# Optimization experiments

Measured on AMD Instinct MI355X. Metric: run time of the kernel, lower is better.

The kernel has to match this reference:

```python
import jax, jax.numpy as jnp
import numpy as np
from jax import lax

B, K, Z, C, H, W = 32, 7, 64, 3, 64, 64
G = H + 6  # decoder grid for 'small' variant
ITERS = 3
SCALE = Z ** -0.5
EPS = 1e-8


def _pe(h, w):
    # matches SlotAttention.create_positional_embedding: shape [w, h, 4]
    ww = jnp.linspace(0.0, 1.0, w)
    hh = jnp.linspace(0.0, 1.0, h)
    a = jnp.broadcast_to((1.0 - ww)[:, None], (w, h))  # dist_right
    b = jnp.broadcast_to(ww[:, None], (w, h))          # dist_left
    c = jnp.broadcast_to(hh[None, :], (w, h))          # dist_top
    d = jnp.broadcast_to((1.0 - hh)[None, :], (w, h))  # dist_bottom
    return jnp.stack([a, b, c, d], -1)


def _ln(x, g, b):
    m = x.mean(-1, keepdims=True)
    v = ((x - m) ** 2).mean(-1, keepdims=True)
    return (x - m) * lax.rsqrt(v + 1e-5) * g + b


def _conv(x, w, b, p):
    y = lax.conv_general_dilated(x, w, (1, 1), [(p, p), (p, p)],
                                 dimension_numbers=('NCHW', 'OIHW', 'NCHW'))
    return y + b[None, :, None, None]


def setup_inputs() -> dict:
    key = jax.random.key(0)
    ks = iter(jax.random.split(key, 64))
    nrm = lambda shape, s=0.05: jax.random.normal(next(ks), shape, jnp.float32) * s
    d = {}
    d['inputs'] = jax.random.normal(next(ks), (B, C, H, W), jnp.float32)
    d['noise'] = jax.random.normal(next(ks), (B * K, Z), jnp.float32)
    d['enc_pos_w'] = nrm((4, 64)); d['enc_pos_b'] = jnp.zeros(64, jnp.float32)
    d['ec1_w'] = nrm((64, 3, 5, 5)); d['ec1_b'] = jnp.zeros(64, jnp.float32)
    d['ec2_w'] = nrm((64, 64, 5, 5)); d['ec2_b'] = jnp.zeros(64, jnp.float32)
    d['ec3_w'] = nrm((64, 64, 5, 5)); d['ec3_b'] = jnp.zeros(64, jnp.float32)
    d['ec4_w'] = nrm((64, 64, 5, 5)); d['ec4_b'] = jnp.zeros(64, jnp.float32)
    d['ln1_g'] = jnp.ones(64, jnp.float32); d['ln1_b'] = jnp.zeros(64, jnp.float32)
    d['fc1_w'] = nrm((64, 64)); d['fc1_b'] = jnp.zeros(64, jnp.float32)
    d['fc2_w'] = nrm((64, 64)); d['fc2_b'] = jnp.zeros(64, jnp.float32)
    d['lns_g'] = jnp.ones(Z, jnp.float32); d['lns_b'] = jnp.zeros(Z, jnp.float32)
    d['lnf_g'] = jnp.ones(Z, jnp.float32); d['lnf_b'] = jnp.zeros(Z, jnp.float32)
    d['q_w'] = nrm((Z, Z)); d['k_w'] = nrm((64, Z)); d['v_w'] = nrm((64, Z))
    d['mlp1_w'] = nrm((Z, 128)); d['mlp1_b'] = jnp.zeros(128, jnp.float32)
    d['mlp2_w'] = nrm((128, Z)); d['mlp2_b'] = jnp.zeros(Z, jnp.float32)
    d['gru_wih'] = nrm((3 * Z, Z)); d['gru_whh'] = nrm((3 * Z, Z))
    d['gru_bih'] = jnp.zeros(3 * Z, jnp.float32); d['gru_bhh'] = jnp.zeros(3 * Z, jnp.float32)
    d['init_slots'] = jnp.concatenate([jnp.zeros((1, Z), jnp.float32), jnp.ones((1, Z), jnp.float32)], 1)
    d['dec_pos_w'] = nrm((4, Z)); d['dec_pos_b'] = jnp.zeros(Z, jnp.float32)
    d['dc1_w'] = nrm((32, Z, 5, 5)); d['dc1_b'] = jnp.zeros(32, jnp.float32)
    d['dc2_w'] = nrm((32, 32, 5, 5)); d['dc2_b'] = jnp.zeros(32, jnp.float32)
    d['dc3_w'] = nrm((32, 32, 5, 5)); d['dc3_b'] = jnp.zeros(32, jnp.float32)
    d['dc4_w'] = nrm((4, 32, 3, 3)); d['dc4_b'] = jnp.zeros(4, jnp.float32)
    return d


def _forward(inputs, noise, enc_pos_w, enc_pos_b, ec1_w, ec1_b, ec2_w, ec2_b,
             ec3_w, ec3_b, ec4_w, ec4_b, ln1_g, ln1_b, fc1_w, fc1_b, fc2_w, fc2_b,
             lns_g, lns_b, lnf_g, lnf_b, q_w, k_w, v_w, mlp1_w, mlp1_b, mlp2_w,
             mlp2_b, gru_wih, gru_whh, gru_bih, gru_bhh, init_slots, dec_pos_w,
             dec_pos_b, dc1_w, dc1_b, dc2_w, dc2_b, dc3_w, dc3_b, dc4_w, dc4_b):
    # ---- encoder ----
    h = jax.nn.relu(_conv(inputs, ec1_w, ec1_b, 2))
    h = jax.nn.relu(_conv(h, ec2_w, ec2_b, 2))
    h = jax.nn.relu(_conv(h, ec3_w, ec3_b, 2))
    h = jax.nn.relu(_conv(h, ec4_w, ec4_b, 2))
    h = h.transpose(0, 2, 3, 1)                        # [B,H,W,64]
    pe = _pe(H, W) @ enc_pos_w + enc_pos_b             # [W,H,64] (H==W)
    h = h + pe[None]
    feat = h.reshape(B, H * W, 64)
    feat = _ln(feat, ln1_g, ln1_b)
    feat = jax.nn.relu(feat @ fc1_w + fc1_b) @ fc2_w + fc2_b
    k = feat @ k_w                                     # [B,N,Z]
    v = feat @ v_w
    # ---- slot init: Normal(loc, softplus(sp)).rsample() ----
    loc, sp = jnp.split(init_slots, 2, axis=1)
    slots = (loc + jax.nn.softplus(sp) * noise).reshape(B, K, Z)
    # ---- iterative slot attention ----
    for _ in range(ITERS):
        prev = slots
        q = (_ln(prev, lns_g, lns_b) @ q_w) * SCALE
        dots = jnp.einsum('bid,bjd->bij', q, k)        # [B,K,N]
        attn = jax.nn.softmax(dots, axis=1) + EPS      # normalize over slots
        attn = attn / attn.sum(-1, keepdims=True)      # renormalize over keys
        updates = jnp.einsum('bjd,bij->bid', v, attn)  # [B,K,Z]
        # GRU cell (single step), torch gate order r,z,n
        gi = updates.reshape(-1, Z) @ gru_wih.T + gru_bih
        gh = prev.reshape(-1, Z) @ gru_whh.T + gru_bhh
        ir, iz, inn = jnp.split(gi, 3, -1)
        hr, hz, hn = jnp.split(gh, 3, -1)
        r = jax.nn.sigmoid(ir + hr)
        zg = jax.nn.sigmoid(iz + hz)
        n = jnp.tanh(inn + r * hn)
        slots = ((1.0 - zg) * n + zg * prev.reshape(-1, Z)).reshape(B, K, Z)
        slots = slots + (jax.nn.relu(_ln(slots, lnf_g, lnf_b) @ mlp1_w + mlp1_b) @ mlp2_w + mlp2_b)
    # ---- spatial-broadcast decoder ('small') ----
    flat = slots.reshape(B * K, Z)
    zb = jnp.broadcast_to(flat[:, :, None, None], (B * K, Z, G, G))
    pe_d = (_pe(G, G) @ dec_pos_w + dec_pos_b).transpose(2, 0, 1)  # [Z,G,G]
    zb = zb + pe_d[None]
    o = jax.nn.relu(_conv(zb, dc1_w, dc1_b, 1))        # 70->68
    o = jax.nn.relu(_conv(o, dc2_w, dc2_b, 1))         # 68->66
    o = jax.nn.relu(_conv(o, dc3_w, dc3_b, 1))         # 66->64
    o = _conv(o, dc4_w, dc4_b, 1)                      # 64->64, 4ch
    x_loc = jax.nn.sigmoid(o[:, :3]).reshape(B, K, C, H, W)
    mask_logits = o[:, 3].reshape(B, K, 1, H, W)
    mask_logp = jax.nn.log_softmax(mask_logits, axis=1)
    x_orig = (inputs + 1.0) / 2.0
    recon = (x_loc * jnp.exp(mask_logp)).sum(1)
    mse = ((x_orig - recon) ** 2).sum() / B
    return mse, x_loc, mask_logp, slots


def reference(inputs, noise, enc_pos_w, enc_pos_b, ec1_w, ec1_b, ec2_w, ec2_b,
              ec3_w, ec3_b, ec4_w, ec4_b, ln1_g, ln1_b, fc1_w, fc1_b, fc2_w, fc2_b,
              lns_g, lns_b, lnf_g, lnf_b, q_w, k_w, v_w, mlp1_w, mlp1_b, mlp2_w,
              mlp2_b, gru_wih, gru_whh, gru_bih, gru_bhh, init_slots, dec_pos_w,
              dec_pos_b, dc1_w, dc1_b, dc2_w, dc2_b, dc3_w, dc3_b, dc4_w, dc4_b):
    return _forward(inputs, noise, enc_pos_w, enc_pos_b, ec1_w, ec1_b, ec2_w, ec2_b,
                    ec3_w, ec3_b, ec4_w, ec4_b, ln1_g, ln1_b, fc1_w, fc1_b, fc2_w, fc2_b,
                    lns_g, lns_b, lnf_g, lnf_b, q_w, k_w, v_w, mlp1_w, mlp1_b, mlp2_w,
                    mlp2_b, gru_wih, gru_whh, gru_bih, gru_bhh, init_slots, dec_pos_w,
                    dec_pos_b, dc1_w, dc1_b, dc2_w, dc2_b, dc3_w, dc3_b, dc4_w, dc4_b)
```

## Files before the change

### kernel.cpp

```cpp
#include <hip/hip_runtime.h>
#include <math.h>

typedef short bf16x8 __attribute__((ext_vector_type(8)));
typedef float f32x4 __attribute__((ext_vector_type(4)));

#define WS_B0   0u
#define WS_B1   4194304u
#define WS_K    8388608u
#define WS_V    16777216u
#define WS_ATTN 25165824u
#define WS_PART 26083328u
#define WS_SLOT 26327040u
#define WS_ROW  26341376u
#define SCALE_ 0.125f

#define OFF_PEB   0u
#define OFF_WCLS  160000u
#define OFF_S     180000u
#define OFF_ZB    250000u

__device__ __forceinline__ float wave_sum(float v) {
#pragma unroll
    for (int m = 32; m >= 1; m >>= 1) v += __shfl_xor(v, m, 64);
    return v;
}
__device__ __forceinline__ unsigned short f2bf(float f) {
    unsigned u = __float_as_uint(f);
    u = u + 0x7fffu + ((u >> 16) & 1u);
    return (unsigned short)(u >> 16);
}
__device__ __forceinline__ float bf2f(unsigned short h) {
    return __uint_as_float(((unsigned)h) << 16);
}

__global__ __launch_bounds__(256) void pack_weights(
    const float* __restrict__ w, unsigned short* __restrict__ wp,
    int CIN, int COUT_STORE, int KS, int NT, int total)
{
    int t = blockIdx.x * 256 + threadIdx.x;
    if (t >= total) return;
    int lane = t & 63;
    int nt = (t >> 6) % NT;
    int ch = t / (64 * NT);
    int CPT = CIN / 32;
    int cic = ch % CPT;
    int tap = ch / CPT;
    int ky = tap / KS, kx = tap % KS;
    int co = nt * 16 + (lane & 15);
    int k0 = cic * 32 + (lane >> 4) * 8;
    unsigned short v[8];
#pragma unroll
    for (int j = 0; j < 8; ++j) {
        int ci = k0 + j;
        float f = (co < COUT_STORE) ? w[((size_t)(co * CIN + ci) * KS + ky) * KS + kx] : 0.f;
        v[j] = f2bf(f);
    }
    *(uint4*)(wp + (size_t)t * 8) = *(uint4*)v;
}

__global__ __launch_bounds__(256) void pack_fc(
    const float* __restrict__ w, unsigned short* __restrict__ wp)
{
    int t = blockIdx.x * 256 + threadIdx.x;
    if (t >= 512) return;
    int lane = t & 63;
    int nt = (t >> 6) & 3;
    int ck = t >> 8;
    int n = nt * 16 + (lane & 15);
    int k0 = ck * 32 + (lane >> 4) * 8;
    unsigned short v[8];
#pragma unroll
    for (int j = 0; j < 8; ++j) v[j] = f2bf(w[(size_t)(k0 + j) * 64 + n]);
    *(uint4*)(wp + (size_t)t * 8) = *(uint4*)v;
}

template<int CIN, int COUT, int KS, int PAD, int NSTORE, int RELU, int OUTF32>
__global__ __launch_bounds__(256) void conv_mfma(
    const unsigned short* __restrict__ in, const unsigned short* __restrict__ wpack,
    const float* __restrict__ bias, void* __restrict__ outv,
    int Hin, int Win, int Hout, int Wout, int tilesX, int tilesY)
{
    constexpr int TS = 16, TH = TS + KS - 1;
    constexpr int NT = COUT / 16;
    constexpr int CPT = CIN / 32;
    constexpr int G8 = CIN / 8;
    __shared__ __align__(16) unsigned short tile[TH][TH][CIN];
    const int tpb = tilesX * tilesY;
    const int n = blockIdx.x / tpb;
    const int t = blockIdx.x % tpb;
    const int ty0 = (t / tilesX) * TS, tx0 = (t % tilesX) * TS;
    const int tid = threadIdx.x;

    const unsigned short* inb = in + (size_t)n * Hin * Win * CIN;
    for (int idx = tid; idx < TH * TH * G8; idx += 256) {
        int g = idx % G8;
        int c = (idx / G8) % TH;
        int r = idx / (G8 * TH);
        int iy = ty0 - PAD + r, ix = tx0 - PAD + c;
        uint4 vv = make_uint4(0, 0, 0, 0);
        if (iy >= 0 && iy < Hin && ix >= 0 && ix < Win)
            vv = *(const uint4*)(inb + ((size_t)iy * Win + ix) * CIN + g * 8);
        int slot = (g * 8 + c * 8) % CIN;
        *(uint4*)&tile[r][c][slot] = vv;
    }
    __syncthreads();

    const int wv = tid >> 6, lane = tid & 63;
    const int q = lane >> 4, m = lane & 15;
    const int row0 = wv * 4;
    f32x4 acc[4][NT];
#pragma unroll
    for (int mt = 0; mt < 4; ++mt)
#pragma unroll
        for (int nt = 0; nt < NT; ++nt) acc[mt][nt] = (f32x4){0.f, 0.f, 0.f, 0.f};

#pragma unroll
    for (int cic = 0; cic < CPT; ++cic) {
#pragma unroll
        for (int kx = 0; kx < KS; ++kx) {
            bf16x8 B[KS][NT];
#pragma unroll
            for (int ky = 0; ky < KS; ++ky)
#pragma unroll
                for (int nt = 0; nt < NT; ++nt)
                    B[ky][nt] = *(const bf16x8*)(wpack +
                        ((size_t)(((ky * KS + kx) * CPT + cic) * NT + nt) * 64 + lane) * 8);
            const int cbase = m + kx;
            const int slot = (cic * 32 + q * 8 + cbase * 8) % CIN;
#pragma unroll
            for (int ir = 0; ir < KS + 3; ++ir) {
                bf16x8 afr = *(const bf16x8*)&tile[row0 + ir][cbase][slot];
#pragma unroll
                for (int ky = 0; ky < KS; ++ky) {
                    const int mt = ir - ky;
                    if (mt < 0 || mt > 3) continue;
#pragma unroll
                    for (int nt = 0; nt < NT; ++nt)
                        acc[mt][nt] = __builtin_amdgcn_mfma_f32_16x16x32_bf16(afr, B[ky][nt], acc[mt][nt], 0, 0, 0);
                }
            }
        }
    }

#pragma unroll
    for (int nt = 0; nt < NT; ++nt) {
        const int co = nt * 16 + m;
        const float bv = (co < NSTORE) ? bias[co] : 0.f;
#pragma unroll
        for (int mt = 0; mt < 4; ++mt) {
            const int oy = ty0 + wv * 4 + mt;
#pragma unroll
            for (int j = 0; j < 4; ++j) {
                const int ox = tx0 + q * 4 + j;
                if (oy < Hout && ox < Wout && co < NSTORE) {
                    float v = acc[mt][nt][j] + bv;
                    if (RELU) v = fmaxf(v, 0.f);
                    size_t o = (((size_t)n * Hout + oy) * Wout + ox) * NSTORE + co;
                    if (OUTF32) ((float*)outv)[o] = v;
                    else ((unsigned short*)outv)[o] = f2bf(v);
                }
            }
        }
    }
}

__global__ __launch_bounds__(256) void pe_synth(
    const float* __restrict__ dpw, const float* __restrict__ dpb,
    unsigned short* __restrict__ peb, float* __restrict__ zbias)
{
    const int tid = threadIdx.x;
    if (blockIdx.x == 0 && tid < 32) zbias[tid] = 0.f;
    const int pix = blockIdx.x * 256 + tid;
    if (pix >= 4900) return;
    const int iy = pix / 70, ix = pix % 70;
    const float fy = iy * (1.f / 69.f), fx = ix * (1.f / 69.f);
    unsigned short v[64];
#pragma unroll
    for (int ci = 0; ci < 64; ++ci) {
        float p = (1.f - fy) * dpw[ci] + fy * dpw[64 + ci]
                + fx * dpw[128 + ci] + (1.f - fx) * dpw[192 + ci] + dpb[ci];
        v[ci] = f2bf(p);
    }
    uint4* ob = (uint4*)(peb + (size_t)pix * 64);
#pragma unroll
    for (int i = 0; i < 8; ++i) ob[i] = ((uint4*)v)[i];
}

__global__ __launch_bounds__(256) void wcls_build(
    const float* __restrict__ w, float* __restrict__ wcls)
{
    int idx = blockIdx.x * 256 + threadIdx.x;
    if (idx >= 9 * 32 * 64) return;
    int cls = idx / (32 * 64);
    int co = (idx / 64) % 32;
    int ci = idx % 64;
    int rc = cls / 3, cc = cls % 3;
    int ky0 = (rc == 0) ? 1 : 0, ky1 = (rc == 2) ? 3 : 4;
    int kx0 = (cc == 0) ? 1 : 0, kx1 = (cc == 2) ? 3 : 4;
    float s = 0.f;
    const float* wb = w + (size_t)(co * 64 + ci) * 25;
    for (int ky = ky0; ky <= ky1; ++ky)
        for (int kx = kx0; kx <= kx1; ++kx)
            s += wb[ky * 5 + kx];
    wcls[idx] = s;
}

__global__ __launch_bounds__(256) void slot_s(
    const float* __restrict__ slots, const float* __restrict__ wcls,
    float* __restrict__ S)
{
    int idx = blockIdx.x * 256 + threadIdx.x;
    if (idx >= 224 * 9 * 32) return;
    int n = idx / (9 * 32);
    int cls = (idx / 32) % 9;
    int co = idx % 32;
    const float* sl = slots + n * 64;
    const float* wc = wcls + (size_t)(cls * 32 + co) * 64;
    float s = 0.f;
#pragma unroll
    for (int ci = 0; ci < 64; ++ci) s = fmaf(sl[ci], wc[ci], s);
    S[idx] = s;
}

__global__ __launch_bounds__(256) void dc1_assemble(
    const float* __restrict__ P, const float* __restrict__ S,
    const float* __restrict__ bias, int n0,
    unsigned short* __restrict__ out)
{
    const int gid = blockIdx.x * 256 + threadIdx.x;
    const int nl = gid / 4624;
    const int pix = gid % 4624;
    const int oy = pix / 68, ox = pix % 68;
    const int rc = (oy == 0) ? 0 : ((oy == 67) ? 2 : 1);
    const int cc = (ox == 0) ? 0 : ((ox == 67) ? 2 : 1);
    const float* Sp = S + ((size_t)(n0 + nl) * 9 + (rc * 3 + cc)) * 32;
    const float* Pp = P + (size_t)pix * 32;
    unsigned short v[32];
#pragma unroll
    for (int co = 0; co < 32; ++co)
        v[co] = f2bf(fmaxf(bias[co] + Pp[co] + Sp[co], 0.f));
    uint4* ob = (uint4*)(out + ((size_t)nl * 4624 + pix) * 32);
#pragma unroll
    for (int i = 0; i < 4; ++i) ob[i] = ((uint4*)v)[i];
}

__global__ __launch_bounds__(256) void conv_ec1(
    const float* __restrict__ in, const float* __restrict__ wts,
    const float* __restrict__ bias, unsigned short* __restrict__ out)
{
    __shared__ float tile[3][20][21];
    const int blk = blockIdx.x;
    const int n = blk >> 6;
    const int sub = blk & 63;
    const int t = sub >> 2;
    const int cog = sub & 3;
    const int ty0 = (t >> 2) * 16, tx0 = (t & 3) * 16;
    const int tid = threadIdx.x;
    for (int idx = tid; idx < 1200; idx += 256) {
        int ci = idx / 400, rc = idx % 400;
        int r = rc / 20, c = rc % 20;
        int gy = ty0 + r - 2, gx = tx0 + c - 2;
        float v = 0.f;
        if (gy >= 0 && gy < 64 && gx >= 0 && gx < 64)
            v = in[((size_t)n * 3 + ci) * 4096 + gy * 64 + gx];
        tile[ci][r][c] = v;
    }
    __syncthreads();
    const int lx = tid & 15, ly = tid >> 4;
    float acc[16];
#pragma unroll
    for (int co = 0; co < 16; ++co) acc[co] = bias[cog * 16 + co];
    for (int ci = 0; ci < 3; ++ci) {
        float val[25];
#pragma unroll
        for (int ky = 0; ky < 5; ++ky)
#pragma unroll
            for (int kx = 0; kx < 5; ++kx) val[ky * 5 + kx] = tile[ci][ly + ky][lx + kx];
#pragma unroll
        for (int co = 0; co < 16; ++co) {
            const float* wc = wts + (size_t)((cog * 16 + co) * 3 + ci) * 25;
            float a = acc[co];
#pragma unroll
            for (int tt = 0; tt < 25; ++tt) a = fmaf(val[tt], wc[tt], a);
            acc[co] = a;
        }
    }
    unsigned short tmp[16];
#pragma unroll
    for (int co = 0; co < 16; ++co) tmp[co] = f2bf(fmaxf(acc[co], 0.f));
    uint4* ob = (uint4*)(out + (((size_t)n * 64 + ty0 + ly) * 64 + tx0 + lx) * 64 + cog * 16);
    ob[0] = ((uint4*)tmp)[0];
    ob[1] = ((uint4*)tmp)[1];
}

__global__ __launch_bounds__(256) void encoder_tail_mfma(
    const unsigned short* __restrict__ h4,
    const float* __restrict__ epw, const float* __restrict__ epb,
    const float* __restrict__ ln1g, const float* __restrict__ ln1b,
    const unsigned short* __restrict__ pfc1, const float* __restrict__ fc1b,
    const unsigned short* __restrict__ pfc2, const float* __restrict__ fc2b,
    const unsigned short* __restrict__ pkw, const unsigned short* __restrict__ pvw,
    unsigned short* __restrict__ kout, unsigned short* __restrict__ vout)
{
    __shared__ __align__(16) unsigned short X[64][72];
    const int b = blockIdx.x >> 6;
    const int y = blockIdx.x & 63;
    const int tid = threadIdx.x;

    {
        const int p = tid >> 2, sub = tid & 3;
        const unsigned short* hp = h4 + ((((size_t)b * 64 + y) * 64 + p) * 64) + sub * 16;
        unsigned short raw[16];
        *(uint4*)(raw)     = *(const uint4*)hp;
        *(uint4*)(raw + 8) = *(const uint4*)(hp + 8);
        const float fy = y * (1.f / 63.f), fx = p * (1.f / 63.f);
        float f[16];
        float s1 = 0.f, s2 = 0.f;
#pragma unroll
        for (int j = 0; j < 16; ++j) {
            int ch = sub * 16 + j;
            float pe = (1.f - fy) * epw[ch] + fy * epw[64 + ch]
                     + fx * epw[128 + ch] + (1.f - fx) * epw[192 + ch] + epb[ch];
            float v = bf2f(raw[j]) + pe;
            f[j] = v;
            s1 += v;
            s2 += v * v;
        }
        s1 += __shfl_xor(s1, 1, 64); s1 += __shfl_xor(s1, 2, 64);
        s2 += __shfl_xor(s2, 1, 64); s2 += __shfl_xor(s2, 2, 64);
        const float m = s1 * (1.f / 64.f);
        const float var = s2 * (1.f / 64.f) - m * m;
        const float inv = rsqrtf(var + 1e-5f);
        unsigned short xb[16];
#pragma unroll
        for (int j = 0; j < 16; ++j) {
            int ch = sub * 16 + j;
            xb[j] = f2bf((f[j] - m) * inv * ln1g[ch] + ln1b[ch]);
        }
        *(uint4*)&X[p][sub * 16]     = ((uint4*)xb)[0];
        *(uint4*)&X[p][sub * 16 + 8] = ((uint4*)xb)[1];
    }
    __syncthreads();

    const int w = tid >> 6, lane = tid & 63;
    const int q = lane >> 4, m_ = lane & 15;
    const int row0 = w * 16;

    {
        f32x4 a1[4];
#pragma unroll
        for (int nt = 0; nt < 4; ++nt) a1[nt] = (f32x4){0.f, 0.f, 0.f, 0.f};
#pragma unroll
        for (int ck = 0; ck < 2; ++ck) {
            bf16x8 afr = *(const bf16x8*)&X[row0 + m_][ck * 32 + q * 8];
#pragma unroll
            for (int nt = 0; nt < 4; ++nt) {
                bf16x8 bfr = *(const bf16x8*)(pfc1 + ((size_t)((ck * 4 + nt) * 64 + lane)) * 8);
                a1[nt] = __builtin_amdgcn_mfma_f32_16x16x32_bf16(afr, bfr, a1[nt], 0, 0, 0);
            }
        }
        __syncthreads();
#pragma unroll
        for (int nt = 0; nt < 4; ++nt) {
            const float bb = fc1b[nt * 16 + m_];
#pragma unroll
            for (int reg = 0; reg < 4; ++reg)
                X[row0 + q * 4 + reg][nt * 16 + m_] = f2bf(fmaxf(a1[nt][reg] + bb, 0.f));
        }
    }
    __syncthreads();

    {
        f32x4 a2[4];
#pragma unroll
        for (int nt = 0; nt < 4; ++nt) a2[nt] = (f32x4){0.f, 0.f, 0.f, 0.f};
#pragma unroll
        for (int ck = 0; ck < 2; ++ck) {
            bf16x8 afr = *(const bf16x8*)&X[row0 + m_][ck * 32 + q * 8];
#pragma unroll
            for (int nt = 0; nt < 4; ++nt) {
                bf16x8 bfr = *(const bf16x8*)(pfc2 + ((size_t)((ck * 4 + nt) * 64 + lane)) * 8);
                a2[nt] = __builtin_amdgcn_mfma_f32_16x16x32_bf16(afr, bfr, a2[nt], 0, 0, 0);
            }
        }
        __syncthreads();
#pragma unroll
        for (int nt = 0; nt < 4; ++nt) {
            const float bb = fc2b[nt * 16 + m_];
#pragma unroll
            for (int reg = 0; reg < 4; ++reg)
                X[row0 + q * 4 + reg][nt * 16 + m_] = f2bf(a2[nt][reg] + bb);
        }
    }
    __syncthreads();

    {
        f32x4 ak[4], av[4];
#pragma unroll
        for (int nt = 0; nt < 4; ++nt) {
            ak[nt] = (f32x4){0.f, 0.f, 0.f, 0.f};
            av[nt] = (f32x4){0.f, 0.f, 0.f, 0.f};
        }
#pragma unroll
        for (int ck = 0; ck < 2; ++ck) {
            bf16x8 afr = *(const bf16x8*)&X[row0 + m_][ck * 32 + q * 8];
#pragma unroll
            for (int nt = 0; nt < 4; ++nt) {
                bf16x8 bk = *(const bf16x8*)(pkw + ((size_t)((ck * 4 + nt) * 64 + lane)) * 8);
                bf16x8 bv = *(const bf16x8*)(pvw + ((size_t)((ck * 4 + nt) * 64 + lane)) * 8);
                ak[nt] = __builtin_amdgcn_mfma_f32_16x16x32_bf16(afr, bk, ak[nt], 0, 0, 0);
                av[nt] = __builtin_amdgcn_mfma_f32_16x16x32_bf16(afr, bv, av[nt], 0, 0, 0);
            }
        }
        const size_t base = ((size_t)b * 4096) + y * 64 + row0;
#pragma unroll
        for (int nt = 0; nt < 4; ++nt) {
            const int ch = nt * 16 + m_;
#pragma unroll
            for (int reg = 0; reg < 4; ++reg) {
                const size_t o = (base + q * 4 + reg) * 64 + ch;
                kout[o] = f2bf(ak[nt][reg]);
                vout[o] = f2bf(av[nt][reg]);
            }
        }
    }
}

__global__ __launch_bounds__(256) void slot_init(
    const float* __restrict__ noise, const float* __restrict__ init_slots,
    float* __restrict__ slots, float* __restrict__ rowsum)
{
    int i = blockIdx.x * 256 + threadIdx.x;
    if (i < 224) rowsum[i] = 0.f;
    if (i < 224 * 64) {
        int z = i & 63;
        float spl = log1pf(expf(init_slots[64 + z]));
        slots[i] = init_slots[z] + spl * noise[i];
    }
}

__global__ __launch_bounds__(256) void attn_pass1(
    const unsigned short* __restrict__ kbuf, const float* __restrict__ slots,
    const float* __restrict__ lnsg, const float* __restrict__ lnsb,
    const float* __restrict__ qw,
    float* __restrict__ attn, float* __restrict__ rowsum)
{
    __shared__ float qs[7][64];
    __shared__ float red[7][4];
    const int b = blockIdx.x >> 4;
    const int jb = (blockIdx.x & 15) * 256;
    const int tid = threadIdx.x;
    const int lane = tid & 63, wv = tid >> 6;
    for (int i = wv; i < 7; i += 4) {
        float s = slots[(b * 7 + i) * 64 + lane];
        float m = wave_sum(s) * (1.f / 64.f);
        float d = s - m;
        float var = wave_sum(d * d) * (1.f / 64.f);
        float x = d * rsqrtf(var + 1e-5f) * lnsg[lane] + lnsb[lane];
        float qv = 0.f;
        for (int c = 0; c < 64; ++c) qv = fmaf(__shfl(x, c, 64), qw[c * 64 + lane], qv);
        qs[i][lane] = qv * SCALE_;
    }
    __syncthreads();
    const int j = jb + tid;
    float kr[64];
    const unsigned short* kp = kbuf + (((size_t)b * 4096) + j) * 64;
#pragma unroll
    for (int d8 = 0; d8 < 8; ++d8) {
        uint4 kv = ((const uint4*)kp)[d8];
        const unsigned short* h = (const unsigned short*)&kv;
#pragma unroll
        for (int z = 0; z < 8; ++z) kr[d8 * 8 + z] = bf2f(h[z]);
    }
    float dots[7];
#pragma unroll
    for (int i = 0; i < 7; ++i) {
        float a = 0.f;
#pragma unroll
        for (int d = 0; d < 64; ++d) a = fmaf(kr[d], qs[i][d], a);
        dots[i] = a;
    }
    float mx = dots[0];
#pragma unroll
    for (int i = 1; i < 7; ++i) mx = fmaxf(mx, dots[i]);
    float sum = 0.f;
#pragma unroll
    for (int i = 0; i < 7; ++i) { dots[i] = expf(dots[i] - mx); sum += dots[i]; }
    const float inv = 1.f / sum;
#pragma unroll
    for (int i = 0; i < 7; ++i) {
        float a = dots[i] * inv + 1e-8f;
        dots[i] = a;
        attn[(((size_t)b * 7) + i) * 4096 + j] = a;
    }
#pragma unroll
    for (int i = 0; i < 7; ++i) {
        float s = wave_sum(dots[i]);
        if (lane == 0) red[i][wv] = s;
    }
    __syncthreads();
    if (tid < 7) {
        float s = red[tid][0] + red[tid][1] + red[tid][2] + red[tid][3];
        atomicAdd(&rowsum[b * 7 + tid], s);
    }
}

__global__ __launch_bounds__(256) void attn_pass2(
    const unsigned short* __restrict__ vbuf, const float* __restrict__ attn,
    float* __restrict__ part)
{
    const int b = blockIdx.x >> 4;
    const int js = blockIdx.x & 15;
    const int tid = threadIdx.x;
    const int d = tid & 63, jc = tid >> 6;
    float acc[7];
#pragma unroll
    for (int i = 0; i < 7; ++i) acc[i] = 0.f;
    const int j0 = js * 256;
    for (int j = j0 + jc; j < j0 + 256; j += 4) {
        float av = bf2f(vbuf[(((size_t)b * 4096) + j) * 64 + d]);
#pragma unroll
        for (int i = 0; i < 7; ++i)
            acc[i] = fmaf(attn[(((size_t)b * 7) + i) * 4096 + j], av, acc[i]);
    }
    __shared__ float red[4][7][64];
#pragma unroll
    for (int i = 0; i < 7; ++i) red[jc][i][d] = acc[i];
    __syncthreads();
    if (tid < 7 * 64) {
        int i = tid / 64, dd = tid % 64;
        float s = red[0][i][dd] + red[1][i][dd] + red[2][i][dd] + red[3][i][dd];
        part[((((size_t)b * 16) + js) * 7 + i) * 64 + dd] = s;
    }
}

__global__ __launch_bounds__(64) void gru_mlp(
    float* __restrict__ slots, const float* __restrict__ part,
    float* __restrict__ rowsum,
    const float* __restrict__ wih, const float* __restrict__ whh,
    const float* __restrict__ bih, const float* __restrict__ bhh,
    const float* __restrict__ lnfg, const float* __restrict__ lnfb,
    const float* __restrict__ m1w, const float* __restrict__ m1b,
    const float* __restrict__ m2w, const float* __restrict__ m2b)
{
    const int n = blockIdx.x;
    const int b = n / 7, i = n % 7;
    const int l = threadIdx.x;
    float upd = 0.f;
    for (int js = 0; js < 16; ++js)
        upd += part[((((size_t)b * 16) + js) * 7 + i) * 64 + l];
    upd /= rowsum[n];
    if (l == 0) rowsum[n] = 0.f;
    const float prev = slots[n * 64 + l];
    float gi0 = bih[l], gi1 = bih[64 + l], gi2 = bih[128 + l];
    float gh0 = bhh[l], gh1 = bhh[64 + l], gh2 = bhh[128 + l];
    for (int c = 0; c < 64; ++c) {
        float u = __shfl(upd, c, 64), p = __shfl(prev, c, 64);
        gi0 = fmaf(u, wih[l * 64 + c], gi0);
        gi1 = fmaf(u, wih[(64 + l) * 64 + c], gi1);
        gi2 = fmaf(u, wih[(128 + l) * 64 + c], gi2);
        gh0 = fmaf(p, whh[l * 64 + c], gh0);
        gh1 = fmaf(p, whh[(64 + l) * 64 + c], gh1);
        gh2 = fmaf(p, whh[(128 + l) * 64 + c], gh2);
    }
    float r  = 1.f / (1.f + expf(-(gi0 + gh0)));
    float zg = 1.f / (1.f + expf(-(gi1 + gh1)));
    float nn = tanhf(gi2 + r * gh2);
    float s = (1.f - zg) * nn + zg * prev;
    float m = wave_sum(s) * (1.f / 64.f);
    float d = s - m;
    float var = wave_sum(d * d) * (1.f / 64.f);
    float x = d * rsqrtf(var + 1e-5f) * lnfg[l] + lnfb[l];
    float h0 = m1b[l], h1 = m1b[64 + l];
    for (int c = 0; c < 64; ++c) {
        float xv = __shfl(x, c, 64);
        h0 = fmaf(xv, m1w[c * 128 + l], h0);
        h1 = fmaf(xv, m1w[c * 128 + 64 + l], h1);
    }
    h0 = fmaxf(h0, 0.f); h1 = fmaxf(h1, 0.f);
    float o = m2b[l];
    for (int c = 0; c < 64; ++c) {
        o = fmaf(__shfl(h0, c, 64), m2w[c * 64 + l], o);
        o = fmaf(__shfl(h1, c, 64), m2w[(64 + c) * 64 + l], o);
    }
    slots[n * 64 + l] = s + o;
}

__global__ __launch_bounds__(256) void finalize_k(
    const float* __restrict__ dc4out, const float* __restrict__ inputs,
    float* __restrict__ out)
{
    const int tid = threadIdx.x;
    const int gp = blockIdx.x * 256 + tid;
    const int b = gp >> 12, p = gp & 4095;
    float4 o4[7];
#pragma unroll
    for (int k = 0; k < 7; ++k)
        o4[k] = ((const float4*)dc4out)[(size_t)(b * 7 + k) * 4096 + p];
    float mx = o4[0].w;
#pragma unroll
    for (int k = 1; k < 7; ++k) mx = fmaxf(mx, o4[k].w);
    float s = 0.f;
#pragma unroll
    for (int k = 0; k < 7; ++k) s += expf(o4[k].w - mx);
    const float lse = mx + logf(s);
    float recon0 = 0.f, recon1 = 0.f, recon2 = 0.f;
    float* xl = out + 1;
    float* ml = out + 2752513;
#pragma unroll
    for (int k = 0; k < 7; ++k) {
        float lp = o4[k].w - lse;
        ml[((size_t)(b * 7 + k)) * 4096 + p] = lp;
        float w = expf(lp);
        float x0 = 1.f / (1.f + expf(-o4[k].x));
        float x1 = 1.f / (1.f + expf(-o4[k].y));
        float x2 = 1.f / (1.f + expf(-o4[k].z));
        xl[(((size_t)(b * 7 + k)) * 3 + 0) * 4096 + p] = x0;
        xl[(((size_t)(b * 7 + k)) * 3 + 1) * 4096 + p] = x1;
        xl[(((size_t)(b * 7 + k)) * 3 + 2) * 4096 + p] = x2;
        recon0 = fmaf(x0, w, recon0);
        recon1 = fmaf(x1, w, recon1);
        recon2 = fmaf(x2, w, recon2);
    }
    float err = 0.f;
    {
        float xo = (inputs[((size_t)b * 3 + 0) * 4096 + p] + 1.f) * 0.5f;
        float dd = xo - recon0; err += dd * dd;
        xo = (inputs[((size_t)b * 3 + 1) * 4096 + p] + 1.f) * 0.5f;
        dd = xo - recon1; err += dd * dd;
        xo = (inputs[((size_t)b * 3 + 2) * 4096 + p] + 1.f) * 0.5f;
        dd = xo - recon2; err += dd * dd;
    }
    float wsum = wave_sum(err);
    __shared__ float red[4];
    const int lane = tid & 63, wv = tid >> 6;
    if (lane == 0) red[wv] = wsum;
    __syncthreads();
    if (tid == 0) atomicAdd(out, (red[0] + red[1] + red[2] + red[3]) * (1.f / 32.f));
}

__global__ __launch_bounds__(256) void copy_slots(const float* __restrict__ slots,
                                                  float* __restrict__ out)
{
    int i = blockIdx.x * 256 + threadIdx.x;
    if (i == 0) out[0] = 0.f;
    if (i < 14336) out[3670017 + i] = slots[i];
}

extern "C" void kernel_launch(void* const* d_in, const int* in_sizes, int n_in,
                              void* d_out, int out_size, void* d_ws, size_t ws_size,
                              hipStream_t stream) {
    (void)in_sizes; (void)n_in; (void)out_size; (void)ws_size;
    const float* inputs = (const float*)d_in[0];
    const float* noise  = (const float*)d_in[1];
    const float* epw  = (const float*)d_in[2];
    const float* epb  = (const float*)d_in[3];
    const float* ec1w = (const float*)d_in[4];
    const float* ec1b = (const float*)d_in[5];
    const float* ec2w = (const float*)d_in[6];
    const float* ec2b = (const float*)d_in[7];
    const float* ec3w = (const float*)d_in[8];
    const float* ec3b = (const float*)d_in[9];
    const float* ec4w = (const float*)d_in[10];
    const float* ec4b = (const float*)d_in[11];
    const float* ln1g = (const float*)d_in[12];
    const float* ln1b = (const float*)d_in[13];
    const float* fc1w = (const float*)d_in[14];
    const float* fc1b = (const float*)d_in[15];
    const float* fc2w = (const float*)d_in[16];
    const float* fc2b = (const float*)d_in[17];
    const float* lnsg = (const float*)d_in[18];
    const float* lnsb = (const float*)d_in[19];
    const float* lnfg = (const float*)d_in[20];
    const float* lnfb = (const float*)d_in[21];
    const float* qw   = (const float*)d_in[22];
    const float* kw   = (const float*)d_in[23];
    const float* vw   = (const float*)d_in[24];
    const float* m1w  = (const float*)d_in[25];
    const float* m1b  = (const float*)d_in[26];
    const float* m2w  = (const float*)d_in[27];
    const float* m2b  = (const float*)d_in[28];
    const float* wih  = (const float*)d_in[29];
    const float* whh  = (const float*)d_in[30];
    const float* bih  = (const float*)d_in[31];
    const float* bhh  = (const float*)d_in[32];
    const float* init_slots = (const float*)d_in[33];
    const float* dpw  = (const float*)d_in[34];
    const float* dpb  = (const float*)d_in[35];
    const float* dc1w = (const float*)d_in[36];
    const float* dc1b = (const float*)d_in[37];
    const float* dc2w = (const float*)d_in[38];
    const float* dc2b = (const float*)d_in[39];
    const float* dc3w = (const float*)d_in[40];
    const float* dc3b = (const float*)d_in[41];
    const float* dc4w = (const float*)d_in[42];
    const float* dc4b = (const float*)d_in[43];

    float* ws = (float*)d_ws;
    unsigned short* B0 = (unsigned short*)(ws + WS_B0);
    unsigned short* B1 = (unsigned short*)(ws + WS_B1);
    unsigned short* K = (unsigned short*)(ws + WS_K);
    unsigned short* V = (unsigned short*)(ws + WS_V);
    unsigned short* dping = (unsigned short*)(ws + WS_B0);
    unsigned short* dpong = (unsigned short*)(ws + WS_K);
    float* dc4out = ws + WS_V;
    unsigned short* PK = (unsigned short*)(ws + WS_V + 4194304u);
    unsigned short* p_ec2 = PK, *p_ec3 = PK + 102400, *p_ec4 = PK + 204800;
    unsigned short* p_dc1 = PK, *p_dc2 = PK + 51200, *p_dc3 = PK + 76800, *p_dc4 = PK + 102400;
    float* attn  = ws + WS_ATTN;
    unsigned short* PFC = (unsigned short*)attn;
    unsigned short* p_fc1 = PFC, *p_fc2 = PFC + 4096, *p_kw = PFC + 8192, *p_vw = PFC + 12288;
    unsigned short* peb = (unsigned short*)(attn + OFF_PEB);
    float* wclsb = attn + OFF_WCLS;
    float* Sbuf  = attn + OFF_S;
    float* zbias = attn + OFF_ZB;
    float* part  = ws + WS_PART;
    float* P     = ws + WS_PART;
    float* slots = ws + WS_SLOT;
    float* rowsum = ws + WS_ROW;
    float* out = (float*)d_out;

    pack_weights<<<50, 256, 0, stream>>>(ec2w, p_ec2, 64, 64, 5, 4, 12800);
    pack_weights<<<50, 256, 0, stream>>>(ec3w, p_ec3, 64, 64, 5, 4, 12800);
    pack_weights<<<50, 256, 0, stream>>>(ec4w, p_ec4, 64, 64, 5, 4, 12800);
    pack_fc<<<2, 256, 0, stream>>>(fc1w, p_fc1);
    pack_fc<<<2, 256, 0, stream>>>(fc2w, p_fc2);
    pack_fc<<<2, 256, 0, stream>>>(kw, p_kw);
    pack_fc<<<2, 256, 0, stream>>>(vw, p_vw);

    conv_ec1<<<2048, 256, 0, stream>>>(inputs, ec1w, ec1b, B0);
    conv_mfma<64, 64, 5, 2, 64, 1, 0><<<512, 256, 0, stream>>>(B0, p_ec2, ec2b, B1, 64, 64, 64, 64, 4, 4);
    conv_mfma<64, 64, 5, 2, 64, 1, 0><<<512, 256, 0, stream>>>(B1, p_ec3, ec3b, B0, 64, 64, 64, 64, 4, 4);
    conv_mfma<64, 64, 5, 2, 64, 1, 0><<<512, 256, 0, stream>>>(B0, p_ec4, ec4b, B1, 64, 64, 64, 64, 4, 4);
    encoder_tail_mfma<<<2048, 256, 0, stream>>>(B1, epw, epb, ln1g, ln1b,
                                                p_fc1, fc1b, p_fc2, fc2b, p_kw, p_vw, K, V);
    slot_init<<<56, 256, 0, stream>>>(noise, init_slots, slots, rowsum);

    for (int it = 0; it < 3; ++it) {
        attn_pass1<<<512, 256, 0, stream>>>(K, slots, lnsg, lnsb, qw, attn, rowsum);
        attn_pass2<<<512, 256, 0, stream>>>(V, attn, part);
        gru_mlp<<<224, 64, 0, stream>>>(slots, part, rowsum, wih, whh, bih, bhh,
                                        lnfg, lnfb, m1w, m1b, m2w, m2b);
    }

    pack_weights<<<25, 256, 0, stream>>>(dc1w, p_dc1, 64, 32, 5, 2, 6400);
    pack_weights<<<13, 256, 0, stream>>>(dc2w, p_dc2, 32, 32, 5, 2, 3200);
    pack_weights<<<13, 256, 0, stream>>>(dc3w, p_dc3, 32, 32, 5, 2, 3200);
    pack_weights<<<3, 256, 0, stream>>>(dc4w, p_dc4, 32, 4, 3, 1, 576);
    pe_synth<<<20, 256, 0, stream>>>(dpw, dpb, peb, zbias);
    conv_mfma<64, 32, 5, 1, 32, 0, 1><<<25, 256, 0, stream>>>(peb, p_dc1, zbias, P, 70, 70, 68, 68, 5, 5);
    wcls_build<<<72, 256, 0, stream>>>(dc1w, wclsb);
    slot_s<<<252, 256, 0, stream>>>(slots, wclsb, Sbuf);

    for (int ch = 0; ch < 2; ++ch) {
        float* d4o = dc4out + (size_t)ch * 112 * 4 * 4096;
        dc1_assemble<<<2023, 256, 0, stream>>>(P, Sbuf, dc1b, ch * 112, dping);
        conv_mfma<32, 32, 5, 1, 32, 1, 0><<<2800, 256, 0, stream>>>(dping, p_dc2, dc2b, dpong, 68, 68, 66, 66, 5, 5);
        conv_mfma<32, 32, 5, 1, 32, 1, 0><<<1792, 256, 0, stream>>>(dpong, p_dc3, dc3b, dping, 66, 66, 64, 64, 4, 4);
        conv_mfma<32, 16, 3, 1, 4, 0, 1><<<1792, 256, 0, stream>>>(dping, p_dc4, dc4b, d4o, 64, 64, 64, 64, 4, 4);
    }

    copy_slots<<<56, 256, 0, stream>>>(slots, out);
    finalize_k<<<512, 256, 0, stream>>>(dc4out, inputs, out);
}
```

Baseline: 763.3 us.

## Fuse attention passes, batch weight packing, split encoder conv output channels

Merges the two attention kernels into one that keeps the attention weights in shared memory, so the global attn write and re-read are gone. Weight-packing launches are combined into single kernels. The encoder convs are split across two output-channel groups per tile, doubling the block count to 1024 with fewer accumulators per block. The shared-memory tile swizzle is also simplified. The channel split reloads each input tile twice, and the fused attention kernel uses more shared memory per block.

```diff
diff --git a/kernel.cpp b/kernel.cpp
--- a/kernel.cpp
+++ b/kernel.cpp
@@ -58,73 +58,111 @@
     *(uint4*)(wp + (size_t)t * 8) = *(uint4*)v;
 }
 
-__global__ __launch_bounds__(256) void pack_fc(
-    const float* __restrict__ w, unsigned short* __restrict__ wp)
+__global__ __launch_bounds__(256) void pack_weights3(
+    const float* __restrict__ w0, const float* __restrict__ w1,
+    const float* __restrict__ w2, unsigned short* __restrict__ wp)
 {
     int t = blockIdx.x * 256 + threadIdx.x;
-    if (t >= 512) return;
-    int lane = t & 63;
-    int nt = (t >> 6) & 3;
-    int ck = t >> 8;
+    if (t >= 38400) return;
+    int which = t / 12800;
+    int tt = t % 12800;
+    const float* w = (which == 0) ? w0 : ((which == 1) ? w1 : w2);
+    unsigned short* dst = wp + (size_t)which * 102400;
+    int lane = tt & 63;
+    int nt = (tt >> 6) & 3;
+    int ch = tt >> 8;
+    int cic = ch & 1;
+    int tap = ch >> 1;
+    int ky = tap / 5, kx = tap % 5;
+    int co = nt * 16 + (lane & 15);
+    int k0 = cic * 32 + (lane >> 4) * 8;
+    unsigned short v[8];
+#pragma unroll
+    for (int j = 0; j < 8; ++j) {
+        int ci = k0 + j;
+        v[j] = f2bf(w[((size_t)(co * 64 + ci) * 5 + ky) * 5 + kx]);
+    }
+    *(uint4*)(dst + (size_t)tt * 8) = *(uint4*)v;
+}
+
+__global__ __launch_bounds__(256) void pack_fc4(
+    const float* __restrict__ w0, const float* __restrict__ w1,
+    const float* __restrict__ w2, const float* __restrict__ w3,
+    unsigned short* __restrict__ wp)
+{
+    int t = blockIdx.x * 256 + threadIdx.x;
+    if (t >= 2048) return;
+    int which = t / 512;
+    int tt = t % 512;
+    const float* w = (which == 0) ? w0 : ((which == 1) ? w1 : ((which == 2) ? w2 : w3));
+    unsigned short* dst = wp + (size_t)which * 4096;
+    int lane = tt & 63;
+    int nt = (tt >> 6) & 3;
+    int ck = tt >> 8;
     int n = nt * 16 + (lane & 15);
     int k0 = ck * 32 + (lane >> 4) * 8;
     unsigned short v[8];
 #pragma unroll
     for (int j = 0; j < 8; ++j) v[j] = f2bf(w[(size_t)(k0 + j) * 64 + n]);
-    *(uint4*)(wp + (size_t)t * 8) = *(uint4*)v;
-}
-
-template<int CIN, int COUT, int KS, int PAD, int NSTORE, int RELU, int OUTF32>
+    *(uint4*)(dst + (size_t)tt * 8) = *(uint4*)v;
+}
+
+template<int CIN, int NTT, int NTU, int KS, int PAD, int NSTORE, int RELU, int OUTF32>
 __global__ __launch_bounds__(256) void conv_mfma(
     const unsigned short* __restrict__ in, const unsigned short* __restrict__ wpack,
     const float* __restrict__ bias, void* __restrict__ outv,
     int Hin, int Win, int Hout, int Wout, int tilesX, int tilesY)
 {
     constexpr int TS = 16, TH = TS + KS - 1;
-    constexpr int NT = COUT / 16;
     constexpr int CPT = CIN / 32;
     constexpr int G8 = CIN / 8;
+    constexpr int CS = NTT / NTU;
     __shared__ __align__(16) unsigned short tile[TH][TH][CIN];
     const int tpb = tilesX * tilesY;
-    const int n = blockIdx.x / tpb;
-    const int t = blockIdx.x % tpb;
+    const int blk = blockIdx.x;
+    const int n = blk / (tpb * CS);
+    const int rem = blk % (tpb * CS);
+    const int t = rem / CS;
+    const int cog = rem % CS;
+    const int ntb = cog * NTU;
     const int ty0 = (t / tilesX) * TS, tx0 = (t % tilesX) * TS;
     const int tid = threadIdx.x;
 
     const unsigned short* inb = in + (size_t)n * Hin * Win * CIN;
     for (int idx = tid; idx < TH * TH * G8; idx += 256) {
-        int g = idx % G8;
-        int c = (idx / G8) % TH;
-        int r = idx / (G8 * TH);
+        const int r = idx / (TH * G8);
+        const int p = idx % (TH * G8);
+        const int c = p / G8;
+        const int chunk = p % G8;
+        const int g = (chunk - c) & (G8 - 1);
         int iy = ty0 - PAD + r, ix = tx0 - PAD + c;
         uint4 vv = make_uint4(0, 0, 0, 0);
         if (iy >= 0 && iy < Hin && ix >= 0 && ix < Win)
             vv = *(const uint4*)(inb + ((size_t)iy * Win + ix) * CIN + g * 8);
-        int slot = (g * 8 + c * 8) % CIN;
-        *(uint4*)&tile[r][c][slot] = vv;
+        *(uint4*)&tile[r][c][chunk * 8] = vv;
     }
     __syncthreads();
 
     const int wv = tid >> 6, lane = tid & 63;
     const int q = lane >> 4, m = lane & 15;
     const int row0 = wv * 4;
-    f32x4 acc[4][NT];
+    f32x4 acc[4][NTU];
 #pragma unroll
     for (int mt = 0; mt < 4; ++mt)
 #pragma unroll
-        for (int nt = 0; nt < NT; ++nt) acc[mt][nt] = (f32x4){0.f, 0.f, 0.f, 0.f};
+        for (int nt = 0; nt < NTU; ++nt) acc[mt][nt] = (f32x4){0.f, 0.f, 0.f, 0.f};
 
 #pragma unroll
     for (int cic = 0; cic < CPT; ++cic) {
 #pragma unroll
         for (int kx = 0; kx < KS; ++kx) {
-            bf16x8 B[KS][NT];
+            bf16x8 B[KS][NTU];
 #pragma unroll
             for (int ky = 0; ky < KS; ++ky)
 #pragma unroll
-                for (int nt = 0; nt < NT; ++nt)
+                for (int nt = 0; nt < NTU; ++nt)
                     B[ky][nt] = *(const bf16x8*)(wpack +
-                        ((size_t)(((ky * KS + kx) * CPT + cic) * NT + nt) * 64 + lane) * 8);
+                        ((size_t)(((ky * KS + kx) * CPT + cic) * NTT + ntb + nt) * 64 + lane) * 8);
             const int cbase = m + kx;
             const int slot = (cic * 32 + q * 8 + cbase * 8) % CIN;
 #pragma unroll
@@ -135,7 +173,7 @@
                     const int mt = ir - ky;
                     if (mt < 0 || mt > 3) continue;
 #pragma unroll
-                    for (int nt = 0; nt < NT; ++nt)
+                    for (int nt = 0; nt < NTU; ++nt)
                         acc[mt][nt] = __builtin_amdgcn_mfma_f32_16x16x32_bf16(afr, B[ky][nt], acc[mt][nt], 0, 0, 0);
                 }
             }
@@ -143,8 +181,8 @@
     }
 
 #pragma unroll
-    for (int nt = 0; nt < NT; ++nt) {
-        const int co = nt * 16 + m;
+    for (int nt = 0; nt < NTU; ++nt) {
+        const int co = (ntb + nt) * 16 + m;
         const float bv = (co < NSTORE) ? bias[co] : 0.f;
 #pragma unroll
         for (int mt = 0; mt < 4; ++mt) {
@@ -439,18 +477,23 @@
     }
 }
 
-__global__ __launch_bounds__(256) void attn_pass1(
-    const unsigned short* __restrict__ kbuf, const float* __restrict__ slots,
+__global__ __launch_bounds__(256) void attn_fused(
+    const unsigned short* __restrict__ kbuf, const unsigned short* __restrict__ vbuf,
+    const float* __restrict__ slots,
     const float* __restrict__ lnsg, const float* __restrict__ lnsb,
     const float* __restrict__ qw,
-    float* __restrict__ attn, float* __restrict__ rowsum)
+    float* __restrict__ part, float* __restrict__ rowsum)
 {
     __shared__ float qs[7][64];
-    __shared__ float red[7][4];
+    __shared__ float ash[256][7];
+    __shared__ float red7[7][4];
+    __shared__ float redv[4][7][64];
     const int b = blockIdx.x >> 4;
-    const int jb = (blockIdx.x & 15) * 256;
+    const int js = blockIdx.x & 15;
+    const int j0 = js * 256;
     const int tid = threadIdx.x;
     const int lane = tid & 63, wv = tid >> 6;
+
     for (int i = wv; i < 7; i += 4) {
         float s = slots[(b * 7 + i) * 64 + lane];
         float m = wave_sum(s) * (1.f / 64.f);
@@ -462,74 +505,67 @@
         qs[i][lane] = qv * SCALE_;
     }
     __syncthreads();
-    const int j = jb + tid;
-    float kr[64];
-    const unsigned short* kp = kbuf + (((size_t)b * 4096) + j) * 64;
-#pragma unroll
-    for (int d8 = 0; d8 < 8; ++d8) {
-        uint4 kv = ((const uint4*)kp)[d8];
-        const unsigned short* h = (const unsigned short*)&kv;
-#pragma unroll
-        for (int z = 0; z < 8; ++z) kr[d8 * 8 + z] = bf2f(h[z]);
-    }
-    float dots[7];
-#pragma unroll
-    for (int i = 0; i < 7; ++i) {
-        float a = 0.f;
-#pragma unroll
-        for (int d = 0; d < 64; ++d) a = fmaf(kr[d], qs[i][d], a);
-        dots[i] = a;
-    }
-    float mx = dots[0];
-#pragma unroll
-    for (int i = 1; i < 7; ++i) mx = fmaxf(mx, dots[i]);
-    float sum = 0.f;
-#pragma unroll
-    for (int i = 0; i < 7; ++i) { dots[i] = expf(dots[i] - mx); sum += dots[i]; }
-    const float inv = 1.f / sum;
-#pragma unroll
-    for (int i = 0; i < 7; ++i) {
-        float a = dots[i] * inv + 1e-8f;
-        dots[i] = a;
-        attn[(((size_t)b * 7) + i) * 4096 + j] = a;
-    }
-#pragma unroll
-    for (int i = 0; i < 7; ++i) {
-        float s = wave_sum(dots[i]);
-        if (lane == 0) red[i][wv] = s;
-    }
-    __syncthreads();
-    if (tid < 7) {
-        float s = red[tid][0] + red[tid][1] + red[tid][2] + red[tid][3];
-        atomicAdd(&rowsum[b * 7 + tid], s);
-    }
-}
-
-__global__ __launch_bounds__(256) void attn_pass2(
-    const unsigned short* __restrict__ vbuf, const float* __restrict__ attn,
-    float* __restrict__ part)
-{
-    const int b = blockIdx.x >> 4;
-    const int js = blockIdx.x & 15;
-    const int tid = threadIdx.x;
-    const int d = tid & 63, jc = tid >> 6;
-    float acc[7];
-#pragma unroll
-    for (int i = 0; i < 7; ++i) acc[i] = 0.f;
-    const int j0 = js * 256;
-    for (int j = j0 + jc; j < j0 + 256; j += 4) {
-        float av = bf2f(vbuf[(((size_t)b * 4096) + j) * 64 + d]);
-#pragma unroll
-        for (int i = 0; i < 7; ++i)
-            acc[i] = fmaf(attn[(((size_t)b * 7) + i) * 4096 + j], av, acc[i]);
-    }
-    __shared__ float red[4][7][64];
-#pragma unroll
-    for (int i = 0; i < 7; ++i) red[jc][i][d] = acc[i];
+
+    {
+        const int j = j0 + tid;
+        float kr[64];
+        const unsigned short* kp = kbuf + (((size_t)b * 4096) + j) * 64;
+#pragma unroll
+        for (int d8 = 0; d8 < 8; ++d8) {
+            uint4 kv = ((const uint4*)kp)[d8];
+            const unsigned short* h = (const unsigned short*)&kv;
+#pragma unroll
+            for (int z = 0; z < 8; ++z) kr[d8 * 8 + z] = bf2f(h[z]);
+        }
+        float dots[7];
+#pragma unroll
+        for (int i = 0; i < 7; ++i) {
+            float a = 0.f;
+#pragma unroll
+            for (int d = 0; d < 64; ++d) a = fmaf(kr[d], qs[i][d], a);
+            dots[i] = a;
+        }
+        float mx = dots[0];
+#pragma unroll
+        for (int i = 1; i < 7; ++i) mx = fmaxf(mx, dots[i]);
+        float sum = 0.f;
+#pragma unroll
+        for (int i = 0; i < 7; ++i) { dots[i] = expf(dots[i] - mx); sum += dots[i]; }
+        const float inv = 1.f / sum;
+#pragma unroll
+        for (int i = 0; i < 7; ++i) {
+            float a = dots[i] * inv + 1e-8f;
+            dots[i] = a;
+            ash[tid][i] = a;
+        }
+#pragma unroll
+        for (int i = 0; i < 7; ++i) {
+            float s = wave_sum(dots[i]);
+            if (lane == 0) red7[i][wv] = s;
+        }
+    }
+    __syncthreads();
+    if (tid < 7)
+        atomicAdd(&rowsum[b * 7 + tid], red7[tid][0] + red7[tid][1] + red7[tid][2] + red7[tid][3]);
+
+    {
+        const int d = lane, jc = wv;
+        float acc[7];
+#pragma unroll
+        for (int i = 0; i < 7; ++i) acc[i] = 0.f;
+        for (int jl = jc; jl < 256; jl += 4) {
+            float av = bf2f(vbuf[(((size_t)b * 4096) + j0 + jl) * 64 + d]);
+#pragma unroll
+            for (int i = 0; i < 7; ++i)
+                acc[i] = fmaf(ash[jl][i], av, acc[i]);
+        }
+#pragma unroll
+        for (int i = 0; i < 7; ++i) redv[jc][i][d] = acc[i];
+    }
     __syncthreads();
     if (tid < 7 * 64) {
         int i = tid / 64, dd = tid % 64;
-        float s = red[0][i][dd] + red[1][i][dd] + red[2][i][dd] + red[3][i][dd];
+        float s = redv[0][i][dd] + redv[1][i][dd] + redv[2][i][dd] + redv[3][i][dd];
         part[((((size_t)b * 16) + js) * 7 + i) * 64 + dd] = s;
     }
 }
@@ -720,25 +756,19 @@
     float* rowsum = ws + WS_ROW;
     float* out = (float*)d_out;
 
-    pack_weights<<<50, 256, 0, stream>>>(ec2w, p_ec2, 64, 64, 5, 4, 12800);
-    pack_weights<<<50, 256, 0, stream>>>(ec3w, p_ec3, 64, 64, 5, 4, 12800);
-    pack_weights<<<50, 256, 0, stream>>>(ec4w, p_ec4, 64, 64, 5, 4, 12800);
-    pack_fc<<<2, 256, 0, stream>>>(fc1w, p_fc1);
-    pack_fc<<<2, 256, 0, stream>>>(fc2w, p_fc2);
-    pack_fc<<<2, 256, 0, stream>>>(kw, p_kw);
-    pack_fc<<<2, 256, 0, stream>>>(vw, p_vw);
+    pack_weights3<<<150, 256, 0, stream>>>(ec2w, ec3w, ec4w, p_ec2);
+    pack_fc4<<<8, 256, 0, stream>>>(fc1w, fc2w, kw, vw, p_fc1);
 
     conv_ec1<<<2048, 256, 0, stream>>>(inputs, ec1w, ec1b, B0);
-    conv_mfma<64, 64, 5, 2, 64, 1, 0><<<512, 256, 0, stream>>>(B0, p_ec2, ec2b, B1, 64, 64, 64, 64, 4, 4);
-    conv_mfma<64, 64, 5, 2, 64, 1, 0><<<512, 256, 0, stream>>>(B1, p_ec3, ec3b, B0, 64, 64, 64, 64, 4, 4);
-    conv_mfma<64, 64, 5, 2, 64, 1, 0><<<512, 256, 0, stream>>>(B0, p_ec4, ec4b, B1, 64, 64, 64, 64, 4, 4);
+    conv_mfma<64, 4, 2, 5, 2, 64, 1, 0><<<1024, 256, 0, stream>>>(B0, p_ec2, ec2b, B1, 64, 64, 64, 64, 4, 4);
+    conv_mfma<64, 4, 2, 5, 2, 64, 1, 0><<<1024, 256, 0, stream>>>(B1, p_ec3, ec3b, B0, 64, 64, 64, 64, 4, 4);
+    conv_mfma<64, 4, 2, 5, 2, 64, 1, 0><<<1024, 256, 0, stream>>>(B0, p_ec4, ec4b, B1, 64, 64, 64, 64, 4, 4);
     encoder_tail_mfma<<<2048, 256, 0, stream>>>(B1, epw, epb, ln1g, ln1b,
                                                 p_fc1, fc1b, p_fc2, fc2b, p_kw, p_vw, K, V);
     slot_init<<<56, 256, 0, stream>>>(noise, init_slots, slots, rowsum);
 
     for (int it = 0; it < 3; ++it) {
-        attn_pass1<<<512, 256, 0, stream>>>(K, slots, lnsg, lnsb, qw, attn, rowsum);
-        attn_pass2<<<512, 256, 0, stream>>>(V, attn, part);
+        attn_fused<<<512, 256, 0, stream>>>(K, V, slots, lnsg, lnsb, qw, part, rowsum);
         gru_mlp<<<224, 64, 0, stream>>>(slots, part, rowsum, wih, whh, bih, bhh,
                                         lnfg, lnfb, m1w, m1b, m2w, m2b);
     }
@@ -748,16 +778,16 @@
     pack_weights<<<13, 256, 0, stream>>>(dc3w, p_dc3, 32, 32, 5, 2, 3200);
     pack_weights<<<3, 256, 0, stream>>>(dc4w, p_dc4, 32, 4, 3, 1, 576);
     pe_synth<<<20, 256, 0, stream>>>(dpw, dpb, peb, zbias);
-    conv_mfma<64, 32, 5, 1, 32, 0, 1><<<25, 256, 0, stream>>>(peb, p_dc1, zbias, P, 70, 70, 68, 68, 5, 5);
+    conv_mfma<64, 2, 2, 5, 1, 32, 0, 1><<<25, 256, 0, stream>>>(peb, p_dc1, zbias, P, 70, 70, 68, 68, 5, 5);
     wcls_build<<<72, 256, 0, stream>>>(dc1w, wclsb);
     slot_s<<<252, 256, 0, stream>>>(slots, wclsb, Sbuf);
 
     for (int ch = 0; ch < 2; ++ch) {
         float* d4o = dc4out + (size_t)ch * 112 * 4 * 4096;
         dc1_assemble<<<2023, 256, 0, stream>>>(P, Sbuf, dc1b, ch * 112, dping);
-        conv_mfma<32, 32, 5, 1, 32, 1, 0><<<2800, 256, 0, stream>>>(dping, p_dc2, dc2b, dpong, 68, 68, 66, 66, 5, 5);
-        conv_mfma<32, 32, 5, 1, 32, 1, 0><<<1792, 256, 0, stream>>>(dpong, p_dc3, dc3b, dping, 66, 66, 64, 64, 4, 4);
-        conv_mfma<32, 16, 3, 1, 4, 0, 1><<<1792, 256, 0, stream>>>(dping, p_dc4, dc4b, d4o, 64, 64, 64, 64, 4, 4);
+        conv_mfma<32, 2, 2, 5, 1, 32, 1, 0><<<2800, 256, 0, stream>>>(dping, p_dc2, dc2b, dpong, 68, 68, 66, 66, 5, 5);
+        conv_mfma<32, 2, 2, 5, 1, 32, 1, 0><<<1792, 256, 0, stream>>>(dpong, p_dc3, dc3b, dping, 66, 66, 64, 64, 4, 4);
+        conv_mfma<32, 1, 1, 3, 1, 4, 0, 1><<<1792, 256, 0, stream>>>(dping, p_dc4, dc4b, d4o, 64, 64, 64, 64, 4, 4);
     }
 
     copy_slots<<<56, 256, 0, stream>>>(slots, out);
```

Result: no change. 771.3 us (+1.1%).
